# Optimization experiments

Hardware: AMD Instinct MI355X
Metric: run time of the kernel (lower is better)

The kernel has to match this reference:

```python
import jax, jax.numpy as jnp
import numpy as np

B, SQ, SK = 2, 2048, 2048
D, H = 1024, 16
HD = D // H              # head_dim = 64
R = 128                  # rel_pos_max_distance
P = 2 * R + 1            # num_pos_ids = 257
RADIUS = 256             # local_attention_radius


def setup_inputs() -> dict:
    key = jax.random.key(0)
    ks = jax.random.split(key, 8)
    s = 0.02
    return {
        "Q": jax.random.normal(ks[0], (B, SQ, D), dtype=jnp.float32),
        "K": jax.random.normal(ks[1], (B, SK, D), dtype=jnp.float32),
        "V": jax.random.normal(ks[2], (B, SK, D), dtype=jnp.float32),
        "Wq": jax.random.normal(ks[3], (D, D), dtype=jnp.float32) * s,
        "Wk": jax.random.normal(ks[4], (D, D), dtype=jnp.float32) * s,
        "Wv": jax.random.normal(ks[5], (D, D), dtype=jnp.float32) * s,
        "Wo": jax.random.normal(ks[6], (D, D), dtype=jnp.float32) * s,
        "E": jax.random.normal(ks[7], (P, D), dtype=jnp.float32) * s,  # rel_embeds
    }


def _split_heads(x, W):
    # bias-free projection then split: B x S x D -> B x H x S x HD
    y = x @ W.T
    b, s, _ = y.shape
    return y.reshape(b, s, H, HD).transpose(0, 2, 1, 3)


def reference(Q, K, V, Wq, Wk, Wv, Wo, E):
    q = _split_heads(Q, Wq)  # B,H,Sq,HD
    k = _split_heads(K, Wk)  # B,H,Sk,HD
    v = _split_heads(V, Wv)  # B,H,Sk,HD

    # rel_embeds reshape matches torch: E[p] viewed as (head_dim, num_heads)
    rel = E.reshape(P, HD, H).transpose(2, 0, 1)           # H,P,HD
    Q_rel = jnp.einsum("bhqd,hpd->bhqp", q, rel)           # B,H,Sq,P

    # slided relative position ids: clip(j - i, -R, R) + R
    i = jnp.arange(SQ)[:, None]
    j = jnp.arange(SK)[None, :]
    rel_ids = jnp.clip(j - i, -R, R) + R                   # Sq,Sk
    rel_shift = jnp.take_along_axis(
        Q_rel, jnp.broadcast_to(rel_ids, (B, H, SQ, SK)), axis=3
    )                                                       # B,H,Sq,Sk

    energy = (jnp.einsum("bhqd,bhkd->bhqk", q, k) + rel_shift) / jnp.sqrt(
        jnp.float32(HD)
    )

    # local attention mask: True = masked (outside window of radius RADIUS)
    mask = jnp.abs(j - i) > RADIUS                          # Sq,Sk
    mask = mask & ~jnp.all(mask, axis=-1, keepdims=True)    # never mask full rows
    energy = jnp.where(mask[None, None], -jnp.inf, energy)

    attn = jax.nn.softmax(energy, axis=-1)                  # B,H,Sq,Sk
    out = jnp.einsum("bhqk,bhkd->bhqd", attn, v)            # B,H,Sq,HD
    # torch: view(B,H,Sq,HD).permute(0,2,3,1).flatten(2,3) -> B,Sq,(HD*H)
    out = out.transpose(0, 2, 3, 1).reshape(B, SQ, D)
    return out @ Wo.T
```

## Files before the change

### kernel.cpp

```cpp
#include <hip/hip_runtime.h>
#include <hip/hip_bf16.h>

#define BATCH 2
#define SQn 2048
#define SKn 2048
#define DMODEL 1024
#define NH 16
#define HD 64
#define NPOS 257
#define RWIN 128
#define RADIUS 256

typedef __attribute__((ext_vector_type(8))) short bf16x8;
typedef __attribute__((ext_vector_type(4))) float f32x4;

static __device__ __forceinline__ unsigned short f2bf(float f) {
    union { float f; unsigned u; } v; v.f = f;
    unsigned r = (v.u + 0x7FFFu + ((v.u >> 16) & 1u)) >> 16;
    return (unsigned short)r;
}
static __device__ __forceinline__ float bf2f(unsigned short b) {
    union { unsigned u; float f; } v; v.u = ((unsigned)b) << 16;
    return v.f;
}

static __device__ __forceinline__ void gl_lds16(const unsigned short* g, unsigned short* l) {
    __builtin_amdgcn_global_load_lds(
        (const __attribute__((address_space(1))) unsigned*)g,
        (__attribute__((address_space(3))) unsigned*)l, 16, 0, 0);
}

__global__ __launch_bounds__(256) void convert_kernel(
    const float* __restrict__ Q, const float* __restrict__ K, const float* __restrict__ V,
    const float* __restrict__ Wq, const float* __restrict__ Wk, const float* __restrict__ Wv,
    const float* __restrict__ Wo,
    unsigned short* __restrict__ xb,
    unsigned short* __restrict__ wb,
    unsigned short* __restrict__ woh)
{
    int i = blockIdx.x * 256 + threadIdx.x;
    if (i < 3145728) {
        int which = i >> 20;
        int off = i & 1048575;
        const float* src = which == 0 ? Q : (which == 1 ? K : V);
        unsigned short* dst = xb + (size_t)which * 4194304;
        float4 v4 = ((const float4*)src)[off];
        ushort4 o4;
        o4.x = f2bf(v4.x); o4.y = f2bf(v4.y); o4.z = f2bf(v4.z); o4.w = f2bf(v4.w);
        ((ushort4*)dst)[off] = o4;
    } else {
        int i2 = i - 3145728;
        int which = i2 >> 18;
        int off = i2 & 262143;
        if (which < 3) {
            const float* src = which == 0 ? Wq : (which == 1 ? Wk : Wv);
            unsigned short* dst = wb + (size_t)which * 1048576;
            float4 v4 = ((const float4*)src)[off];
            ushort4 o4;
            o4.x = f2bf(v4.x); o4.y = f2bf(v4.y); o4.z = f2bf(v4.z); o4.w = f2bf(v4.w);
            ((ushort4*)dst)[off] = o4;
        } else {
            float4 v4 = ((const float4*)Wo)[off];
            int e0 = off * 4;
            int n  = e0 >> 10;
            int c0 = e0 & 1023;
            int d  = c0 >> 4;
            int h0 = c0 & 15;
            woh[((size_t)(h0 + 0) * 1024 + n) * 64 + d] = f2bf(v4.x);
            woh[((size_t)(h0 + 1) * 1024 + n) * 64 + d] = f2bf(v4.y);
            woh[((size_t)(h0 + 2) * 1024 + n) * 64 + d] = f2bf(v4.z);
            woh[((size_t)(h0 + 3) * 1024 + n) * 64 + d] = f2bf(v4.w);
        }
    }
}

__global__ __launch_bounds__(256) void mfma_gemm(
    const unsigned short* __restrict__ Xall,
    const unsigned short* __restrict__ Wall,
    unsigned short* __restrict__ Yall)
{
    __shared__ unsigned short S[16384];

    const int tid  = threadIdx.x;
    const int wv   = tid >> 6;
    const int lane = tid & 63;
    const int quad = lane >> 4;
    const int l15  = lane & 15;
    const int z    = blockIdx.z;
    const int m0   = blockIdx.x * 128;
    const int n0   = blockIdx.y * 128;
    const int wr   = (wv >> 1) * 64;
    const int wc   = (wv & 1) * 64;

    const unsigned short* X = Xall + (size_t)z * (4096 * 1024);
    const unsigned short* W = Wall + (size_t)z * (1024 * 1024);

    int srow[2], scol[2];
#pragma unroll
    for (int it = 0; it < 2; ++it) {
        int f = it * 256 + tid;
        srow[it] = f >> 2;
        scol[it] = ((f & 3) ^ ((srow[it] >> 1) & 3)) * 8;
    }

    int aoff[4], boff[4];
#pragma unroll
    for (int t = 0; t < 4; ++t) {
        int R = wr + t * 16 + l15;
        aoff[t] = R * 32 + ((quad ^ ((R >> 1) & 3)) * 8);
        int C = wc + t * 16 + l15;
        boff[t] = C * 32 + ((quad ^ ((C >> 1) & 3)) * 8);
    }

    f32x4 acc[4][4];
#pragma unroll
    for (int i = 0; i < 4; ++i)
#pragma unroll
        for (int j = 0; j < 4; ++j)
            acc[i][j] = (f32x4){0.f, 0.f, 0.f, 0.f};

#pragma unroll
    for (int it = 0; it < 2; ++it) {
        int f = it * 256 + tid;
        gl_lds16(X + (size_t)(m0 + srow[it]) * 1024 + scol[it], &S[f * 8]);
        gl_lds16(W + (size_t)(n0 + srow[it]) * 1024 + scol[it], &S[8192 + f * 8]);
    }

    for (int k0 = 0; k0 < 1024; k0 += 32) {
        const int cur = (k0 >> 5) & 1;
        __syncthreads();

        if (k0 + 32 < 1024) {
            const int nxt = cur ^ 1;
            const int kn = k0 + 32;
#pragma unroll
            for (int it = 0; it < 2; ++it) {
                int f = it * 256 + tid;
                gl_lds16(X + (size_t)(m0 + srow[it]) * 1024 + kn + scol[it],
                         &S[nxt * 4096 + f * 8]);
                gl_lds16(W + (size_t)(n0 + srow[it]) * 1024 + kn + scol[it],
                         &S[8192 + nxt * 4096 + f * 8]);
            }
        }

        const unsigned short* bA = &S[cur * 4096];
        const unsigned short* bB = &S[8192 + cur * 4096];
        bf16x8 a[4], b[4];
#pragma unroll
        for (int t = 0; t < 4; ++t) a[t] = *(const bf16x8*)&bA[aoff[t]];
#pragma unroll
        for (int t = 0; t < 4; ++t) b[t] = *(const bf16x8*)&bB[boff[t]];
#pragma unroll
        for (int i = 0; i < 4; ++i)
#pragma unroll
            for (int j = 0; j < 4; ++j)
                acc[i][j] = __builtin_amdgcn_mfma_f32_16x16x32_bf16(a[i], b[j], acc[i][j], 0, 0, 0);
    }

    unsigned short* Y = Yall + (size_t)z * (4096 * 1024);
    const int b_ = m0 >> 11;
    const int s0 = m0 & (SQn - 1);

    if (z < 2) {
#pragma unroll
        for (int i = 0; i < 4; ++i) {
            int mbase = s0 + wr + i * 16 + quad * 4;
#pragma unroll
            for (int j = 0; j < 4; ++j) {
                int col = n0 + wc + j * 16 + l15;
                int h = col >> 6, dd = col & 63;
                unsigned short* yb = Y + (((size_t)(b_ * NH + h) * SQn) << 6) + dd;
#pragma unroll
                for (int r = 0; r < 4; ++r)
                    yb[(size_t)(mbase + r) << 6] = f2bf(acc[i][j][r]);
            }
        }
    } else {
        unsigned short* const sT = S;
#pragma unroll
        for (int hh = 0; hh < 2; ++hh) {
            __syncthreads();
            if ((wv & 1) == hh) {
#pragma unroll
                for (int i = 0; i < 4; ++i) {
                    int mloc = wr + i * 16 + quad * 4;
#pragma unroll
                    for (int j = 0; j < 4; ++j) {
                        ushort4 pk;
                        pk.x = f2bf(acc[i][j][0]);
                        pk.y = f2bf(acc[i][j][1]);
                        pk.z = f2bf(acc[i][j][2]);
                        pk.w = f2bf(acc[i][j][3]);
                        *(ushort4*)&sT[(j * 16 + l15) * 136 + mloc] = pk;
                    }
                }
            }
            __syncthreads();
            int h = (n0 >> 6) + hh;
            unsigned short* yb = Y + ((size_t)(b_ * NH + h) * HD) * SKn + s0;
#pragma unroll
            for (int it = 0; it < 4; ++it) {
                int u = it * 256 + tid;
                int dd = u >> 4, mc = u & 15;
                uint4 val = *(const uint4*)&sT[dd * 136 + mc * 8];
                *(uint4*)(yb + (size_t)dd * SKn + mc * 8) = val;
            }
        }
    }
}

__global__ __launch_bounds__(256) void gemm_out(
    const unsigned short* __restrict__ aoh,
    const unsigned short* __restrict__ woh,
    float* __restrict__ Y)
{
    __shared__ unsigned short S[24576];

    const int tid  = threadIdx.x;
    const int wv   = tid >> 6;
    const int lane = tid & 63;
    const int quad = lane >> 4;
    const int l15  = lane & 15;
    const int m0   = blockIdx.x * 64;
    const int n0   = blockIdx.y * 128;
    const int wr   = (wv >> 1) * 32;
    const int wc   = (wv & 1) * 64;
    const int b_   = m0 >> 11;
    const int s0   = m0 & (SQn - 1);

    int rowa[2], ca[2];
#pragma unroll
    for (int it = 0; it < 2; ++it) {
        int f = it * 256 + tid;
        rowa[it] = f >> 3;
        ca[it]   = ((f & 7) ^ (rowa[it] & 7)) * 8;
    }
    int rowb[4], cb[4];
#pragma unroll
    for (int it = 0; it < 4; ++it) {
        int f = it * 256 + tid;
        rowb[it] = f >> 3;
        cb[it]   = ((f & 7) ^ (rowb[it] & 7)) * 8;
    }

    int aoff[2][2], boff[2][4];
#pragma unroll
    for (int ks = 0; ks < 2; ++ks) {
#pragma unroll
        for (int i = 0; i < 2; ++i) {
            int R = wr + i * 16 + l15;
            aoff[ks][i] = R * 64 + ((((ks << 2) + quad) ^ (R & 7)) * 8);
        }
#pragma unroll
        for (int j = 0; j < 4; ++j) {
            int C = wc + j * 16 + l15;
            boff[ks][j] = C * 64 + ((((ks << 2) + quad) ^ (C & 7)) * 8);
        }
    }

    f32x4 acc[2][4];
#pragma unroll
    for (int i = 0; i < 2; ++i)
#pragma unroll
        for (int j = 0; j < 4; ++j)
            acc[i][j] = (f32x4){0.f, 0.f, 0.f, 0.f};

    {
        const unsigned short* Ah = aoh + ((size_t)(b_ * NH) * SQn + s0) * HD;
        const unsigned short* Bh = woh + (size_t)n0 * HD;
#pragma unroll
        for (int it = 0; it < 2; ++it)
            gl_lds16(Ah + (size_t)rowa[it] * HD + ca[it], &S[(it * 256 + tid) * 8]);
#pragma unroll
        for (int it = 0; it < 4; ++it)
            gl_lds16(Bh + (size_t)rowb[it] * HD + cb[it], &S[8192 + (it * 256 + tid) * 8]);
    }

    for (int h = 0; h < NH; ++h) {
        const int cur = h & 1;
        __syncthreads();

        if (h + 1 < NH) {
            const int nxt = cur ^ 1;
            const unsigned short* Ah = aoh + ((size_t)(b_ * NH + h + 1) * SQn + s0) * HD;
            const unsigned short* Bh = woh + ((size_t)(h + 1) * 1024 + n0) * HD;
#pragma unroll
            for (int it = 0; it < 2; ++it)
                gl_lds16(Ah + (size_t)rowa[it] * HD + ca[it],
                         &S[nxt * 4096 + (it * 256 + tid) * 8]);
#pragma unroll
            for (int it = 0; it < 4; ++it)
                gl_lds16(Bh + (size_t)rowb[it] * HD + cb[it],
                         &S[8192 + nxt * 8192 + (it * 256 + tid) * 8]);
        }

        const unsigned short* bA = &S[cur * 4096];
        const unsigned short* bB = &S[8192 + cur * 8192];

        bf16x8 a0[2], b0[4];
#pragma unroll
        for (int i = 0; i < 2; ++i) a0[i] = *(const bf16x8*)&bA[aoff[0][i]];
#pragma unroll
        for (int j = 0; j < 4; ++j) b0[j] = *(const bf16x8*)&bB[boff[0][j]];
#pragma unroll
        for (int i = 0; i < 2; ++i)
#pragma unroll
            for (int j = 0; j < 4; ++j)
                acc[i][j] = __builtin_amdgcn_mfma_f32_16x16x32_bf16(a0[i], b0[j], acc[i][j], 0, 0, 0);

        bf16x8 a1[2], b1[4];
#pragma unroll
        for (int i = 0; i < 2; ++i) a1[i] = *(const bf16x8*)&bA[aoff[1][i]];
#pragma unroll
        for (int j = 0; j < 4; ++j) b1[j] = *(const bf16x8*)&bB[boff[1][j]];
#pragma unroll
        for (int i = 0; i < 2; ++i)
#pragma unroll
            for (int j = 0; j < 4; ++j)
                acc[i][j] = __builtin_amdgcn_mfma_f32_16x16x32_bf16(a1[i], b1[j], acc[i][j], 0, 0, 0);
    }

#pragma unroll
    for (int i = 0; i < 2; ++i) {
        int mbase = m0 + wr + i * 16 + quad * 4;
#pragma unroll
        for (int j = 0; j < 4; ++j) {
            int col = n0 + wc + j * 16 + l15;
#pragma unroll
            for (int r = 0; r < 4; ++r)
                Y[(size_t)(mbase + r) * DMODEL + col] = acc[i][j][r];
        }
    }
}

__global__ __launch_bounds__(256) void relt_kernel(
    const float* __restrict__ E, unsigned short* __restrict__ relTb)
{
    int idx = blockIdx.x * 256 + threadIdx.x;
    const int total = NH * NPOS * HD;
    if (idx < total) {
        int d = idx & (HD - 1);
        int p = (idx >> 6) % NPOS;
        int h = idx / (NPOS * HD);
        relTb[idx] = f2bf(E[(size_t)p * DMODEL + d * NH + h]);
    }
}

#define BIAS_S2 0.0014089565402528222f
#define SC2     0.1803368801111204f

__global__ __launch_bounds__(256, 2) void attn_mfma(
    const unsigned short* __restrict__ q,
    const unsigned short* __restrict__ k,
    const unsigned short* __restrict__ vT,
    const unsigned short* __restrict__ relTb,
    unsigned short* __restrict__ aoh)
{
    __shared__ unsigned short sK[64 * 64];
    __shared__ unsigned short sVt[64 * 64];
    __shared__ unsigned short sP[4][16 * 72];
    __shared__ signed char    sq8[128 * 260];
    unsigned short* const sQ = (unsigned short*)sq8;

    const int tid  = threadIdx.x;
    const int w    = tid >> 6;
    const int lane = tid & 63;
    const int quad = lane >> 4;
    const int l15  = lane & 15;
    const int xcd  = blockIdx.x & 7;
    const int sidx = blockIdx.x >> 3;
    const int bh   = (xcd << 2) | (sidx >> 4);
    const int q0   = (sidx & 15) << 7;
    const int h    = bh & (NH - 1);

    const int f1 = tid,       row1 = f1 >> 3;
    const int c1 = ((f1 & 7) ^ (row1 & 7)) * 8;
    const int f2 = 256 + tid, row2 = f2 >> 3;
    const int c2 = ((f2 & 7) ^ (row2 & 7)) * 8;

    {
        const unsigned short* gq = q + ((size_t)bh * SQn + q0) * HD;
#pragma unroll
        for (int it = 0; it < 4; ++it) {
            int f = it * 256 + tid;
            int row = f >> 3;
            int c = ((f & 7) ^ (row & 7)) * 8;
            gl_lds16(gq + row * HD + c, &sQ[f * 8]);
        }
    }
    __syncthreads();

    const int qrow = w * 16 + l15;
    const int qs = (quad ^ (qrow & 7)) * 8;
    bf16x8 a0A = *(const bf16x8*)&sQ[qrow * 64 + qs];
    bf16x8 a1A = *(const bf16x8*)&sQ[qrow * 64 + (qs ^ 32)];
    bf16x8 a0B = *(const bf16x8*)&sQ[(64 + qrow) * 64 + qs];
    bf16x8 a1B = *(const bf16x8*)&sQ[(64 + qrow) * 64 + (qs ^ 32)];

    const int myrow = w * 16 + quad * 4;
    for (int c5 = 0; c5 < 5; ++c5) {
        __syncthreads();
        const unsigned short* gr = relTb + ((size_t)h * NPOS + c5 * 64) * HD;
        gl_lds16(gr + row1 * HD + c1, &sK[f1 * 8]);
        gl_lds16(gr + row2 * HD + c2, &sK[f2 * 8]);
        __syncthreads();
#pragma unroll
        for (int t = 0; t < 4; ++t) {
            int prow = t * 16 + l15;
            int ks = (quad ^ (prow & 7)) * 8;
            bf16x8 b0 = *(const bf16x8*)&sK[prow * 64 + ks];
            bf16x8 b1 = *(const bf16x8*)&sK[prow * 64 + (ks ^ 32)];
            f32x4 ccA = {0.f, 0.f, 0.f, 0.f};
            ccA = __builtin_amdgcn_mfma_f32_16x16x32_bf16(a0A, b0, ccA, 0, 0, 0);
            ccA = __builtin_amdgcn_mfma_f32_16x16x32_bf16(a1A, b1, ccA, 0, 0, 0);
            f32x4 ccB = {0.f, 0.f, 0.f, 0.f};
            ccB = __builtin_amdgcn_mfma_f32_16x16x32_bf16(a0B, b0, ccB, 0, 0, 0);
            ccB = __builtin_amdgcn_mfma_f32_16x16x32_bf16(a1B, b1, ccB, 0, 0, 0);
            int pos = c5 * 64 + t * 16 + l15;
            if (pos < NPOS) {
#pragma unroll
                for (int r = 0; r < 4; ++r) {
                    int iqA = (int)rintf(ccA[r] * 128.0f);
                    iqA = iqA < -127 ? -127 : (iqA > 127 ? 127 : iqA);
                    sq8[(myrow + r) * 260 + pos] = (signed char)iqA;
                    int iqB = (int)rintf(ccB[r] * 128.0f);
                    iqB = iqB < -127 ? -127 : (iqB > 127 ? 127 : iqB);
                    sq8[(64 + myrow + r) * 260 + pos] = (signed char)iqB;
                }
            }
        }
    }
    __syncthreads();

    float bias0A[4], bias256A[4], bias0B[4], bias256B[4];
#pragma unroll
    for (int r = 0; r < 4; ++r) {
        bias0A[r]   = (float)sq8[(myrow + r) * 260 + 0]          * BIAS_S2;
        bias256A[r] = (float)sq8[(myrow + r) * 260 + 256]        * BIAS_S2;
        bias0B[r]   = (float)sq8[(64 + myrow + r) * 260 + 0]     * BIAS_S2;
        bias256B[r] = (float)sq8[(64 + myrow + r) * 260 + 256]   * BIAS_S2;
    }

    const int lo = (q0 - RADIUS) > 0 ? (q0 - RADIUS) : 0;
    const int hi = (q0 + 127 + RADIUS) < (SKn - 1) ? (q0 + 127 + RADIUS) : (SKn - 1);
    const int nt = ((hi - lo) >> 6) + 1;
    const int e_ = l15 - quad * 4;

    const unsigned short* kg = k  + (size_t)bh * SKn * HD;
    const unsigned short* vg = vT + (size_t)bh * HD * SKn;

    float laccA[4] = {0.f, 0.f, 0.f, 0.f};
    float laccB[4] = {0.f, 0.f, 0.f, 0.f};
    f32x4 oA[4], oB[4];
#pragma unroll
    for (int t = 0; t < 4; ++t) {
        oA[t] = (f32x4){0.f, 0.f, 0.f, 0.f};
        oB[t] = (f32x4){0.f, 0.f, 0.f, 0.f};
    }

    {
        gl_lds16(kg + (size_t)(lo + row1) * HD + c1, &sK[f1 * 8]);
        gl_lds16(kg + (size_t)(lo + row2) * HD + c2, &sK[f2 * 8]);
        gl_lds16(vg + (size_t)row1 * SKn + lo + c1, &sVt[f1 * 8]);
        gl_lds16(vg + (size_t)row2 * SKn + lo + c2, &sVt[f2 * 8]);
    }

    for (int kt = 0; kt < nt; ++kt) {
        const int kb = lo + (kt << 6);
        __syncthreads();

        bf16x8 kf0[4], kf1[4], vf0[4], vf1[4];
#pragma unroll
        for (int t = 0; t < 4; ++t) {
            int prow = t * 16 + l15;
            int ks = (quad ^ (prow & 7)) * 8;
            kf0[t] = *(const bf16x8*)&sK[prow * 64 + ks];
            kf1[t] = *(const bf16x8*)&sK[prow * 64 + (ks ^ 32)];
            vf0[t] = *(const bf16x8*)&sVt[prow * 64 + ks];
            vf1[t] = *(const bf16x8*)&sVt[prow * 64 + (ks ^ 32)];
        }
        __syncthreads();

        if (kt + 1 < nt) {
            const int kb2 = kb + 64;
            gl_lds16(kg + (size_t)(kb2 + row1) * HD + c1, &sK[f1 * 8]);
            gl_lds16(kg + (size_t)(kb2 + row2) * HD + c2, &sK[f2 * 8]);
            gl_lds16(vg + (size_t)row1 * SKn + kb2 + c1, &sVt[f1 * 8]);
            gl_lds16(vg + (size_t)row2 * SKn + kb2 + c2, &sVt[f2 * 8]);
        }

        const int dtbaseA = kb - q0 - w * 16;
        if (dtbaseA > -320 && dtbaseA < 272) {
#pragma unroll
            for (int t = 0; t < 4; ++t) {
                const int dt = dtbaseA + t * 16;
                const int spb = (quad * 4) * 72 + t * 16 + l15;
                if (dt <= -272 || dt >= 272) {
#pragma unroll
                    for (int r = 0; r < 4; ++r) sP[w][spb + r * 72] = 0;
                } else {
                    f32x4 sc = {0.f, 0.f, 0.f, 0.f};
                    sc = __builtin_amdgcn_mfma_f32_16x16x32_bf16(a0A, kf0[t], sc, 0, 0, 0);
                    sc = __builtin_amdgcn_mfma_f32_16x16x32_bf16(a1A, kf1[t], sc, 0, 0, 0);

                    float pv[4];
                    if (dt >= -112 && dt <= 112) {
                        int idx0 = myrow * 260 + dt + 128 + e_;
#pragma unroll
                        for (int r = 0; r < 4; ++r) {
                            float bf = (float)sq8[idx0 + r * 259] * BIAS_S2;
                            pv[r] = __builtin_amdgcn_exp2f(fmaf(sc[r], SC2, bf));
                        }
                    } else if (dt >= -240 && dt <= -144) {
#pragma unroll
                        for (int r = 0; r < 4; ++r)
                            pv[r] = __builtin_amdgcn_exp2f(fmaf(sc[r], SC2, bias0A[r]));
                    } else if (dt >= 144 && dt <= 240) {
#pragma unroll
                        for (int r = 0; r < 4; ++r)
                            pv[r] = __builtin_amdgcn_exp2f(fmaf(sc[r], SC2, bias256A[r]));
                    } else {
#pragma unroll
                        for (int r = 0; r < 4; ++r) {
                            int d = dt + e_ - r;
                            bool in = (unsigned)(d + RADIUS) <= 2u * RADIUS;
                            int p = d < -RWIN ? 0 : (d > RWIN ? 2 * RWIN : d + RWIN);
                            float bf = (float)sq8[(myrow + r) * 260 + p] * BIAS_S2;
                            float e = __builtin_amdgcn_exp2f(fmaf(sc[r], SC2, bf));
                            pv[r] = in ? e : 0.0f;
                        }
                    }
#pragma unroll
                    for (int r = 0; r < 4; ++r) {
                        unsigned short pb = f2bf(pv[r]);
                        sP[w][spb + r * 72] = pb;
                        laccA[r] += bf2f(pb);
                    }
                }
            }
            bf16x8 p0 = *(const bf16x8*)&sP[w][l15 * 72 + quad * 8];
            bf16x8 p1 = *(const bf16x8*)&sP[w][l15 * 72 + 32 + quad * 8];
#pragma unroll
            for (int t = 0; t < 4; ++t) {
                oA[t] = __builtin_amdgcn_mfma_f32_16x16x32_bf16(p0, vf0[t], oA[t], 0, 0, 0);
                oA[t] = __builtin_amdgcn_mfma_f32_16x16x32_bf16(p1, vf1[t], oA[t], 0, 0, 0);
            }
        }

        const int dtbaseB = dtbaseA - 64;
        if (dtbaseB > -320 && dtbaseB < 272) {
#pragma unroll
            for (int t = 0; t < 4; ++t) {
                const int dt = dtbaseB + t * 16;
                const int spb = (quad * 4) * 72 + t * 16 + l15;
                if (dt <= -272 || dt >= 272) {
#pragma unroll
                    for (int r = 0; r < 4; ++r) sP[w][spb + r * 72] = 0;
                } else {
                    f32x4 sc = {0.f, 0.f, 0.f, 0.f};
                    sc = __builtin_amdgcn_mfma_f32_16x16x32_bf16(a0B, kf0[t], sc, 0, 0, 0);
                    sc = __builtin_amdgcn_mfma_f32_16x16x32_bf16(a1B, kf1[t], sc, 0, 0, 0);

                    float pv[4];
                    if (dt >= -112 && dt <= 112) {
                        int idx0 = (64 + myrow) * 260 + dt + 128 + e_;
#pragma unroll
                        for (int r = 0; r < 4; ++r) {
                            float bf = (float)sq8[idx0 + r * 259] * BIAS_S2;
                            pv[r] = __builtin_amdgcn_exp2f(fmaf(sc[r], SC2, bf));
                        }
                    } else if (dt >= -240 && dt <= -144) {
#pragma unroll
                        for (int r = 0; r < 4; ++r)
                            pv[r] = __builtin_amdgcn_exp2f(fmaf(sc[r], SC2, bias0B[r]));
                    } else if (dt >= 144 && dt <= 240) {
#pragma unroll
                        for (int r = 0; r < 4; ++r)
                            pv[r] = __builtin_amdgcn_exp2f(fmaf(sc[r], SC2, bias256B[r]));
                    } else {
#pragma unroll
                        for (int r = 0; r < 4; ++r) {
                            int d = dt + e_ - r;
                            bool in = (unsigned)(d + RADIUS) <= 2u * RADIUS;
                            int p = d < -RWIN ? 0 : (d > RWIN ? 2 * RWIN : d + RWIN);
                            float bf = (float)sq8[(64 + myrow + r) * 260 + p] * BIAS_S2;
                            float e = __builtin_amdgcn_exp2f(fmaf(sc[r], SC2, bf));
                            pv[r] = in ? e : 0.0f;
                        }
                    }
#pragma unroll
                    for (int r = 0; r < 4; ++r) {
                        unsigned short pb = f2bf(pv[r]);
                        sP[w][spb + r * 72] = pb;
                        laccB[r] += bf2f(pb);
                    }
                }
            }
            bf16x8 p0 = *(const bf16x8*)&sP[w][l15 * 72 + quad * 8];
            bf16x8 p1 = *(const bf16x8*)&sP[w][l15 * 72 + 32 + quad * 8];
#pragma unroll
            for (int t = 0; t < 4; ++t) {
                oB[t] = __builtin_amdgcn_mfma_f32_16x16x32_bf16(p0, vf0[t], oB[t], 0, 0, 0);
                oB[t] = __builtin_amdgcn_mfma_f32_16x16x32_bf16(p1, vf1[t], oB[t], 0, 0, 0);
            }
        }
    }

    float linvA[4], linvB[4];
#pragma unroll
    for (int r = 0; r < 4; ++r) {
        float lA = laccA[r];
        float lB = laccB[r];
#pragma unroll
        for (int off = 1; off <= 8; off <<= 1) {
            lA += __shfl_xor(lA, off);
            lB += __shfl_xor(lB, off);
        }
        linvA[r] = 1.0f / lA;
        linvB[r] = 1.0f / lB;
    }

    unsigned short* ob = aoh + ((size_t)bh * SQn + q0) * HD;
#pragma unroll
    for (int t = 0; t < 4; ++t) {
#pragma unroll
        for (int r = 0; r < 4; ++r) {
            int irow = w * 16 + quad * 4 + r;
            ob[irow * HD + t * 16 + l15] = f2bf(oA[t][r] * linvA[r]);
            ob[(64 + irow) * HD + t * 16 + l15] = f2bf(oB[t][r] * linvB[r]);
        }
    }
}

extern "C" void kernel_launch(void* const* d_in, const int* in_sizes, int n_in,
                              void* d_out, int out_size, void* d_ws, size_t ws_size,
                              hipStream_t stream) {
    const float* Q  = (const float*)d_in[0];
    const float* K  = (const float*)d_in[1];
    const float* V  = (const float*)d_in[2];
    const float* Wq = (const float*)d_in[3];
    const float* Wk = (const float*)d_in[4];
    const float* Wv = (const float*)d_in[5];
    const float* Wo = (const float*)d_in[6];
    const float* E  = (const float*)d_in[7];
    float* out = (float*)d_out;

    char* p = (char*)d_ws;
    unsigned short* xb    = (unsigned short*)p; p += (size_t)24 << 20;
    unsigned short* wb    = (unsigned short*)p; p += (size_t)6  << 20;
    unsigned short* woh   = (unsigned short*)p; p += (size_t)2  << 20;
    unsigned short* head  = (unsigned short*)p; p += (size_t)24 << 20;
    unsigned short* relTb = (unsigned short*)p; p += (size_t)1  << 20;
    unsigned short* aoh   = (unsigned short*)p;

    unsigned short* qb  = head;
    unsigned short* kb  = head + 4194304;
    unsigned short* vTb = head + 8388608;

    dim3 bb(256);
    convert_kernel<<<dim3(16384), bb, 0, stream>>>(Q, K, V, Wq, Wk, Wv, Wo, xb, wb, woh);
    relt_kernel<<<dim3(1028), bb, 0, stream>>>(E, relTb);
    mfma_gemm<<<dim3(32, 8, 3), bb, 0, stream>>>(xb, wb, head);
    attn_mfma<<<dim3(BATCH * NH * (SQn / 128)), bb, 0, stream>>>(qb, kb, vTb, relTb, aoh);
    gemm_out<<<dim3(64, 8), bb, 0, stream>>>(aoh, woh, out);
}
```

Measured before the change: 208.8 us.

## Single-buffer GEMM staging, change LDS swizzle, raise wave priority around PV MFMAs

The projection GEMM's LDS staging goes from double-buffered prefetch to a single buffer. It now loads and syncs, then computes each k-step, and uses a different XOR swizzle function. The transpose scratch gets its own shared array instead of aliasing the staging buffer. In the attention kernel, s_setprio brackets the P·V MFMA blocks so those waves get issue priority. Dropping the double buffering removes the overlap of global loads with MFMA work, which exposes load latency, in exchange for less LDS and a simpler schedule.

```diff
diff --git a/kernel.cpp b/kernel.cpp
--- a/kernel.cpp
+++ b/kernel.cpp
@@ -29,6 +29,8 @@
         (const __attribute__((address_space(1))) unsigned*)g,
         (__attribute__((address_space(3))) unsigned*)l, 16, 0, 0);
 }
+
+#define SWZ(row) (((row) ^ ((row) >> 2)) & 3)
 
 __global__ __launch_bounds__(256) void convert_kernel(
     const float* __restrict__ Q, const float* __restrict__ K, const float* __restrict__ V,
@@ -79,7 +81,9 @@
     const unsigned short* __restrict__ Wall,
     unsigned short* __restrict__ Yall)
 {
-    __shared__ unsigned short S[16384];
+    __shared__ unsigned short sA[128 * 32];
+    __shared__ unsigned short sB[128 * 32];
+    __shared__ unsigned short sT[64 * 136];
 
     const int tid  = threadIdx.x;
     const int wv   = tid >> 6;
@@ -95,21 +99,22 @@
     const unsigned short* X = Xall + (size_t)z * (4096 * 1024);
     const unsigned short* W = Wall + (size_t)z * (1024 * 1024);
 
-    int srow[2], scol[2];
-#pragma unroll
-    for (int it = 0; it < 2; ++it) {
-        int f = it * 256 + tid;
-        srow[it] = f >> 2;
-        scol[it] = ((f & 3) ^ ((srow[it] >> 1) & 3)) * 8;
-    }
-
     int aoff[4], boff[4];
 #pragma unroll
     for (int t = 0; t < 4; ++t) {
-        int R = wr + t * 16 + l15;
-        aoff[t] = R * 32 + ((quad ^ ((R >> 1) & 3)) * 8);
-        int C = wc + t * 16 + l15;
-        boff[t] = C * 32 + ((quad ^ ((C >> 1) & 3)) * 8);
+        int row = wr + t * 16 + l15;
+        aoff[t] = row * 32 + ((quad ^ SWZ(row)) * 8);
+        int col = wc + t * 16 + l15;
+        boff[t] = col * 32 + ((quad ^ SWZ(col)) * 8);
+    }
+
+    int srow[2], scg[2], sf[2];
+#pragma unroll
+    for (int r = 0; r < 2; ++r) {
+        int f = r * 256 + tid;
+        sf[r] = f;
+        srow[r] = f >> 2;
+        scg[r] = (f & 3) ^ SWZ(srow[r]);
     }
 
     f32x4 acc[4][4];
@@ -119,42 +124,25 @@
         for (int j = 0; j < 4; ++j)
             acc[i][j] = (f32x4){0.f, 0.f, 0.f, 0.f};
 
-#pragma unroll
-    for (int it = 0; it < 2; ++it) {
-        int f = it * 256 + tid;
-        gl_lds16(X + (size_t)(m0 + srow[it]) * 1024 + scol[it], &S[f * 8]);
-        gl_lds16(W + (size_t)(n0 + srow[it]) * 1024 + scol[it], &S[8192 + f * 8]);
-    }
-
     for (int k0 = 0; k0 < 1024; k0 += 32) {
-        const int cur = (k0 >> 5) & 1;
         __syncthreads();
-
-        if (k0 + 32 < 1024) {
-            const int nxt = cur ^ 1;
-            const int kn = k0 + 32;
-#pragma unroll
-            for (int it = 0; it < 2; ++it) {
-                int f = it * 256 + tid;
-                gl_lds16(X + (size_t)(m0 + srow[it]) * 1024 + kn + scol[it],
-                         &S[nxt * 4096 + f * 8]);
-                gl_lds16(W + (size_t)(n0 + srow[it]) * 1024 + kn + scol[it],
-                         &S[8192 + nxt * 4096 + f * 8]);
-            }
-        }
-
-        const unsigned short* bA = &S[cur * 4096];
-        const unsigned short* bB = &S[8192 + cur * 4096];
-        bf16x8 a[4], b[4];
-#pragma unroll
-        for (int t = 0; t < 4; ++t) a[t] = *(const bf16x8*)&bA[aoff[t]];
-#pragma unroll
-        for (int t = 0; t < 4; ++t) b[t] = *(const bf16x8*)&bB[boff[t]];
+#pragma unroll
+        for (int r = 0; r < 2; ++r) {
+            gl_lds16(X + (size_t)(m0 + srow[r]) * 1024 + k0 + scg[r] * 8, &sA[sf[r] * 8]);
+            gl_lds16(W + (size_t)(n0 + srow[r]) * 1024 + k0 + scg[r] * 8, &sB[sf[r] * 8]);
+        }
+        __syncthreads();
+
+        bf16x8 af[4], bfr[4];
+#pragma unroll
+        for (int t = 0; t < 4; ++t) af[t]  = *(const bf16x8*)&sA[aoff[t]];
+#pragma unroll
+        for (int t = 0; t < 4; ++t) bfr[t] = *(const bf16x8*)&sB[boff[t]];
 #pragma unroll
         for (int i = 0; i < 4; ++i)
 #pragma unroll
             for (int j = 0; j < 4; ++j)
-                acc[i][j] = __builtin_amdgcn_mfma_f32_16x16x32_bf16(a[i], b[j], acc[i][j], 0, 0, 0);
+                acc[i][j] = __builtin_amdgcn_mfma_f32_16x16x32_bf16(af[i], bfr[j], acc[i][j], 0, 0, 0);
     }
 
     unsigned short* Y = Yall + (size_t)z * (4096 * 1024);
@@ -176,7 +164,6 @@
             }
         }
     } else {
-        unsigned short* const sT = S;
 #pragma unroll
         for (int hh = 0; hh < 2; ++hh) {
             __syncthreads();
@@ -540,11 +527,13 @@
             }
             bf16x8 p0 = *(const bf16x8*)&sP[w][l15 * 72 + quad * 8];
             bf16x8 p1 = *(const bf16x8*)&sP[w][l15 * 72 + 32 + quad * 8];
+            __builtin_amdgcn_s_setprio(1);
 #pragma unroll
             for (int t = 0; t < 4; ++t) {
                 oA[t] = __builtin_amdgcn_mfma_f32_16x16x32_bf16(p0, vf0[t], oA[t], 0, 0, 0);
                 oA[t] = __builtin_amdgcn_mfma_f32_16x16x32_bf16(p1, vf1[t], oA[t], 0, 0, 0);
             }
+            __builtin_amdgcn_s_setprio(0);
         }
 
         const int dtbaseB = dtbaseA - 64;
@@ -598,11 +587,13 @@
             }
             bf16x8 p0 = *(const bf16x8*)&sP[w][l15 * 72 + quad * 8];
             bf16x8 p1 = *(const bf16x8*)&sP[w][l15 * 72 + 32 + quad * 8];
+            __builtin_amdgcn_s_setprio(1);
 #pragma unroll
             for (int t = 0; t < 4; ++t) {
                 oB[t] = __builtin_amdgcn_mfma_f32_16x16x32_bf16(p0, vf0[t], oB[t], 0, 0, 0);
                 oB[t] = __builtin_amdgcn_mfma_f32_16x16x32_bf16(p1, vf1[t], oB[t], 0, 0, 0);
             }
+            __builtin_amdgcn_s_setprio(0);
         }
     }
 
```

After: 198.2 us. -5.1%, faster.
